# Performance work log

Measured on AMD Instinct MI355X. Metric: run time of the kernel, lower is better.

## Reference

```python
import jax, jax.numpy as jnp
import numpy as np

N_NODES = 50000
N_EDGES = 600000
D = 128
N_GRAPHS = 64


def setup_inputs() -> dict:
    key = jax.random.key(0)
    ks = jax.random.split(key, 16)
    x = jax.random.normal(ks[0], (N_NODES, D), dtype=jnp.float32)
    edge_index = jax.random.randint(ks[1], (2, N_EDGES), 0, N_NODES, dtype=jnp.int64)
    batch = jnp.sort(jax.random.randint(ks[2], (N_NODES,), 0, N_GRAPHS, dtype=jnp.int64))
    s = 1.0 / np.sqrt(D)
    def lin(k, out_d, in_d):
        return jax.random.uniform(k, (out_d, in_d), jnp.float32, -s, s)
    inp = {"x": x, "edge_index": edge_index, "batch": batch}
    for i, base in zip(range(3), (3, 6, 9)):
        inp[f"W_rel{i+1}"] = lin(ks[base], D, D)
        inp[f"b_rel{i+1}"] = jax.random.uniform(ks[base + 1], (D,), jnp.float32, -s, s)
        inp[f"W_root{i+1}"] = lin(ks[base + 2], D, D)
    s5 = 1.0 / np.sqrt(5)
    inp["W1"] = lin(ks[12], 5, D)
    inp["b1"] = jax.random.uniform(ks[13], (5,), jnp.float32, -s, s)
    inp["W2"] = jax.random.uniform(ks[14], (1, 5), jnp.float32, -s5, s5)
    inp["b2"] = jax.random.uniform(ks[15], (1,), jnp.float32, -s5, s5)
    return inp


def graph_conv(x, src, dst, W_rel, b_rel, W_root):
    # PyG GraphConv: out_i = W_root x_i + W_rel * sum_{j->i} x_j + b_rel
    agg = jax.ops.segment_sum(x[src], dst, num_segments=N_NODES)  # [N, D]
    return agg @ W_rel.T + b_rel + x @ W_root.T


def reference(x, edge_index, batch,
              W_rel1, b_rel1, W_root1,
              W_rel2, b_rel2, W_root2,
              W_rel3, b_rel3, W_root3,
              W1, b1, W2, b2):
    src, dst = edge_index[0], edge_index[1]
    h = jax.nn.relu(graph_conv(x, src, dst, W_rel1, b_rel1, W_root1))
    h = jax.nn.relu(graph_conv(h, src, dst, W_rel2, b_rel2, W_root2))
    h = graph_conv(h, src, dst, W_rel3, b_rel3, W_root3)
    # global max pool over graphs
    g = jax.ops.segment_max(h, batch, num_segments=N_GRAPHS)  # [G, D]
    out = jax.nn.relu(g @ W1.T + b1) @ W2.T + b2  # [G, 1]
    return out
```

## Files before the change

kernel.cpp:

```cpp
#include <hip/hip_runtime.h>
#include <float.h>

#define N_NODES 50000
#define N_EDGES 600000
#define D 128
#define N_GRAPHS 64
#define SCAN_T 256
#define SCAN_NBLK ((N_NODES + SCAN_T - 1) / SCAN_T)

typedef __attribute__((ext_vector_type(8))) short short8;
typedef __attribute__((ext_vector_type(4))) float floatx4;

__device__ inline float bf2f(unsigned short h) {
    return __uint_as_float((unsigned)h << 16);
}
__device__ inline unsigned short f2bf(float f) {
    unsigned u = __float_as_uint(f);
    return (unsigned short)((u + 0x7fffu + ((u >> 16) & 1u)) >> 16);
}

#define ACCQ(u, ss) {                                                            \
    int w0_ = (u).x, w1_ = (u).y, w2_ = (u).z, w3_ = (u).w;                      \
    a[ 0] += (float)(signed char)(w0_      ) * (ss);                             \
    a[ 1] += (float)(signed char)(w0_ >>  8) * (ss);                             \
    a[ 2] += (float)(signed char)(w0_ >> 16) * (ss);                             \
    a[ 3] += (float)(w0_ >> 24)              * (ss);                             \
    a[ 4] += (float)(signed char)(w1_      ) * (ss);                             \
    a[ 5] += (float)(signed char)(w1_ >>  8) * (ss);                             \
    a[ 6] += (float)(signed char)(w1_ >> 16) * (ss);                             \
    a[ 7] += (float)(w1_ >> 24)              * (ss);                             \
    a[ 8] += (float)(signed char)(w2_      ) * (ss);                             \
    a[ 9] += (float)(signed char)(w2_ >>  8) * (ss);                             \
    a[10] += (float)(signed char)(w2_ >> 16) * (ss);                             \
    a[11] += (float)(w2_ >> 24)              * (ss);                             \
    a[12] += (float)(signed char)(w3_      ) * (ss);                             \
    a[13] += (float)(signed char)(w3_ >>  8) * (ss);                             \
    a[14] += (float)(signed char)(w3_ >> 16) * (ss);                             \
    a[15] += (float)(w3_ >> 24)              * (ss); }


__global__ __launch_bounds__(256) void cast_prep(
    const float* __restrict__ x,
    unsigned short* __restrict__ xb, signed char* __restrict__ xq,
    float* __restrict__ xs,
    const float* __restrict__ Wr0, const float* __restrict__ Wo0,
    const float* __restrict__ Wr1, const float* __restrict__ Wo1,
    const float* __restrict__ Wr2, const float* __restrict__ Wo2,
    unsigned short* __restrict__ B0, unsigned short* __restrict__ B1,
    unsigned short* __restrict__ B2,
    int* __restrict__ deg, float* __restrict__ g)
{
    int t = blockIdx.x * 256 + threadIdx.x;
    if (t < N_NODES * 16) {
        int node = t >> 4, ln = t & 15;
        const float4* xr = (const float4*)(x + (size_t)node * D + ln * 8);
        float4 v0 = xr[0], v1 = xr[1];
        float v[8] = {v0.x, v0.y, v0.z, v0.w, v1.x, v1.y, v1.z, v1.w};
        float am = 0.f;
#pragma unroll
        for (int i = 0; i < 8; ++i) am = fmaxf(am, fabsf(v[i]));
#pragma unroll
        for (int m = 1; m < 16; m <<= 1) am = fmaxf(am, __shfl_xor(am, m, 16));
        float inv = (am > 0.f) ? 127.f / am : 0.f;
        short8 hb;
#pragma unroll
        for (int i = 0; i < 8; ++i) hb[i] = (short)f2bf(v[i]);
        *(short8*)(xb + (size_t)node * D + ln * 8) = hb;
        int q0 = 0, q1 = 0;
#pragma unroll
        for (int i = 0; i < 4; ++i) { int q = (int)rintf(v[i]     * inv); q0 |= (q & 0xff) << (8 * i); }
#pragma unroll
        for (int i = 0; i < 4; ++i) { int q = (int)rintf(v[4 + i] * inv); q1 |= (q & 0xff) << (8 * i); }
        int2 qp; qp.x = q0; qp.y = q1;
        *(int2*)(xq + (size_t)node * D + ln * 8) = qp;
        if (ln == 0) xs[node] = am * (1.f / 127.f);
        return;
    }
    int w = t - N_NODES * 16;
    if (w < 3 * 128 * 256) {
        int l = w >> 15;
        int r = w & 32767;
        int o = r >> 8, k = r & 255;
        const float* Wr = (l == 0) ? Wr0 : (l == 1) ? Wr1 : Wr2;
        const float* Wo = (l == 0) ? Wo0 : (l == 1) ? Wo1 : Wo2;
        unsigned short* B = (l == 0) ? B0 : (l == 1) ? B1 : B2;
        float v = (k < 128) ? Wr[o * 128 + k] : Wo[o * 128 + (k - 128)];
        B[r] = f2bf(v);
        return;
    }
    w -= 3 * 128 * 256;
    if (w < N_NODES) { deg[w] = 0; return; }
    w -= N_NODES;
    if (w < N_GRAPHS * D) g[w] = -FLT_MAX;
}


__global__ void count_deg(const int* __restrict__ ei, int* __restrict__ deg) {
    int e = blockIdx.x * 256 + threadIdx.x;
    if (e < N_EDGES) atomicAdd(&deg[ei[N_EDGES + e]], 1);
}

__global__ __launch_bounds__(SCAN_T) void block_sum(const int* __restrict__ deg,
                                                    int* __restrict__ blockSums) {
    __shared__ int s[SCAN_T];
    int tid = threadIdx.x;
    int i = blockIdx.x * SCAN_T + tid;
    s[tid] = (i < N_NODES) ? deg[i] : 0;
    __syncthreads();
    for (int off = SCAN_T / 2; off > 0; off >>= 1) {
        if (tid < off) s[tid] += s[tid + off];
        __syncthreads();
    }
    if (tid == 0) blockSums[blockIdx.x] = s[0];
}

__global__ __launch_bounds__(SCAN_T) void scan_write(const int* __restrict__ deg,
                                                     const int* __restrict__ blockSums,
                                                     int* __restrict__ row_start,
                                                     int* __restrict__ cursor) {
    __shared__ int bs[SCAN_T];
    __shared__ int s[SCAN_T];
    int tid = threadIdx.x;
    bs[tid] = (tid < SCAN_NBLK) ? blockSums[tid] : 0;
    __syncthreads();
    for (int off = 1; off < SCAN_T; off <<= 1) {
        int tt = (tid >= off) ? bs[tid - off] : 0;
        __syncthreads();
        bs[tid] += tt;
        __syncthreads();
    }
    int myOff = (blockIdx.x == 0) ? 0 : bs[blockIdx.x - 1];
    if (blockIdx.x == 0 && tid == SCAN_T - 1) row_start[N_NODES] = bs[tid];

    int i = blockIdx.x * SCAN_T + tid;
    int v = (i < N_NODES) ? deg[i] : 0;
    s[tid] = v;
    __syncthreads();
    for (int off = 1; off < SCAN_T; off <<= 1) {
        int tt = (tid >= off) ? s[tid - off] : 0;
        __syncthreads();
        s[tid] += tt;
        __syncthreads();
    }
    if (i < N_NODES) {
        int rs = myOff + s[tid] - v;
        row_start[i] = rs;
        cursor[i]    = rs;
    }
}

__global__ void fill_csr(const int* __restrict__ ei, int* __restrict__ cursor,
                         int* __restrict__ csr_src) {
    int e = blockIdx.x * 256 + threadIdx.x;
    if (e < N_EDGES) {
        int dst = ei[N_EDGES + e];
        int pos = atomicAdd(&cursor[dst], 1);
        csr_src[pos] = ei[e];
    }
}


__global__ __launch_bounds__(256) void gather_q(
    const signed char* __restrict__ xq, const float* __restrict__ xs,
    const int* __restrict__ row_start, const int* __restrict__ csr_src,
    unsigned short* __restrict__ aggb)
{
    int grp  = threadIdx.x >> 3;
    int ln   = threadIdx.x & 7;
    int node = blockIdx.x * 32 + grp;
    if (node >= N_NODES) return;
    int beg = row_start[node];
    int end = row_start[node + 1];

    float a[16];
#pragma unroll
    for (int i = 0; i < 16; ++i) a[i] = 0.f;

    for (int base = beg; base < end; base += 8) {
        int n = end - base; if (n > 8) n = 8;
        int idx = (ln < n) ? csr_src[base + ln] : 0;
        int j = 0;
        for (; j + 3 < n; j += 4) {
            int s0 = __shfl(idx, j,     8); int s1 = __shfl(idx, j + 1, 8);
            int s2 = __shfl(idx, j + 2, 8); int s3 = __shfl(idx, j + 3, 8);
            int4 u0 = *(const int4*)(xq + (size_t)s0 * D + ln * 16);
            int4 u1 = *(const int4*)(xq + (size_t)s1 * D + ln * 16);
            int4 u2 = *(const int4*)(xq + (size_t)s2 * D + ln * 16);
            int4 u3 = *(const int4*)(xq + (size_t)s3 * D + ln * 16);
            float ss0 = xs[s0], ss1 = xs[s1], ss2 = xs[s2], ss3 = xs[s3];
            ACCQ(u0, ss0); ACCQ(u1, ss1); ACCQ(u2, ss2); ACCQ(u3, ss3);
        }
        for (; j < n; ++j) {
            int s0 = __shfl(idx, j, 8);
            int4 u0 = *(const int4*)(xq + (size_t)s0 * D + ln * 16);
            float ss0 = xs[s0];
            ACCQ(u0, ss0);
        }
    }
    short8 r0, r1;
#pragma unroll
    for (int i = 0; i < 8; ++i) { r0[i] = (short)f2bf(a[i]); r1[i] = (short)f2bf(a[8 + i]); }
    *(short8*)(aggb + (size_t)node * D + ln * 16)     = r0;
    *(short8*)(aggb + (size_t)node * D + ln * 16 + 8) = r1;
}


__device__ inline void stage_b_half(unsigned short* sB, const unsigned short* __restrict__ Bb,
                                    int tid, int h) {
#pragma unroll
    for (int i = 0; i < 8; ++i) {
        int flat = tid + i * 256;
        int fi = flat >> 6, ln = flat & 63;
        int mm = ln & 15, qq = ln >> 4;
        int ksL = fi >> 3, tt = fi & 7;
        short8 v = *(const short8*)(Bb + (size_t)(tt * 16 + mm) * 256
                                    + (h * 4 + ksL) * 32 + qq * 8);
        *(short8*)(sB + (size_t)flat * 8) = v;
    }
}


struct GemmShared {
    union {
        unsigned short b[16384];
        float c[64 * 130];
    };
};

__global__ __launch_bounds__(256) void gemm_mfma(
    const unsigned short* __restrict__ aggb, const unsigned short* __restrict__ xb,
    const unsigned short* __restrict__ Bb, const float* __restrict__ bias,
    unsigned short* __restrict__ Ob, signed char* __restrict__ Oq,
    float* __restrict__ Os)
{
    __shared__ GemmShared sh;
    int tid  = threadIdx.x;
    int wave = tid >> 6;
    int lane = tid & 63;
    int m    = lane & 15;
    int quad = lane >> 4;
    int row0 = blockIdx.x * 64 + wave * 16;

    int arow = row0 + m;
    if (arow > N_NODES - 1) arow = N_NODES - 1;

    short8 af[8];
#pragma unroll
    for (int ks = 0; ks < 8; ++ks) {
        const unsigned short* Asrc = (ks < 4) ? aggb : xb;
        af[ks] = *(const short8*)(Asrc + (size_t)arow * 128 + (ks & 3) * 32 + quad * 8);
    }

    floatx4 acc[8];
#pragma unroll
    for (int t = 0; t < 8; ++t) acc[t] = (floatx4){0.f, 0.f, 0.f, 0.f};

    stage_b_half(sh.b, Bb, tid, 0);
    __syncthreads();
#pragma unroll
    for (int ksL = 0; ksL < 4; ++ksL)
#pragma unroll
        for (int t = 0; t < 8; ++t) {
            short8 b = *(const short8*)(sh.b + (size_t)((ksL * 8 + t) * 64 + lane) * 8);
            acc[t] = __builtin_amdgcn_mfma_f32_16x16x32_bf16(af[ksL], b, acc[t], 0, 0, 0);
        }
    __syncthreads();
    stage_b_half(sh.b, Bb, tid, 1);
    __syncthreads();
#pragma unroll
    for (int ksL = 0; ksL < 4; ++ksL)
#pragma unroll
        for (int t = 0; t < 8; ++t) {
            short8 b = *(const short8*)(sh.b + (size_t)((ksL * 8 + t) * 64 + lane) * 8);
            acc[t] = __builtin_amdgcn_mfma_f32_16x16x32_bf16(af[4 + ksL], b, acc[t], 0, 0, 0);
        }
    __syncthreads();

#pragma unroll
    for (int t = 0; t < 8; ++t) {
        int col = t * 16 + m;
        float bv = bias[col];
#pragma unroll
        for (int r = 0; r < 4; ++r) {
            float v = fmaxf(acc[t][r] + bv, 0.f);
            sh.c[(wave * 16 + quad * 4 + r) * 130 + col] = v;
        }
    }
    __syncthreads();

    int lr  = tid >> 2;
    int seg = tid & 3;
    int grow = blockIdx.x * 64 + lr;
    const float* cp = &sh.c[lr * 130 + seg * 32];
    float vv[32];
    float am = 0.f;
#pragma unroll
    for (int i = 0; i < 32; ++i) { vv[i] = cp[i]; am = fmaxf(am, fabsf(vv[i])); }
    am = fmaxf(am, __shfl_xor(am, 1));
    am = fmaxf(am, __shfl_xor(am, 2));
    float inv = (am > 0.f) ? 127.f / am : 0.f;

    if (grow < N_NODES) {
#pragma unroll
        for (int c8 = 0; c8 < 4; ++c8) {
            short8 hb;
#pragma unroll
            for (int i = 0; i < 8; ++i) hb[i] = (short)f2bf(vv[c8 * 8 + i]);
            *(short8*)(Ob + (size_t)grow * 128 + seg * 32 + c8 * 8) = hb;
        }
        int qd[8];
#pragma unroll
        for (int d = 0; d < 8; ++d) {
            int q = 0;
#pragma unroll
            for (int i = 0; i < 4; ++i) {
                int qq = (int)rintf(vv[d * 4 + i] * inv);
                q |= (qq & 0xff) << (8 * i);
            }
            qd[d] = q;
        }
        int4 p0; p0.x = qd[0]; p0.y = qd[1]; p0.z = qd[2]; p0.w = qd[3];
        int4 p1; p1.x = qd[4]; p1.y = qd[5]; p1.z = qd[6]; p1.w = qd[7];
        *(int4*)(Oq + (size_t)grow * 128 + seg * 32)      = p0;
        *(int4*)(Oq + (size_t)grow * 128 + seg * 32 + 16) = p1;
        if (seg == 0) Os[grow] = am * (1.f / 127.f);
    }
}


struct PoolShared {
    union {
        unsigned short b[16384];
        float c[64 * 129];
    };
};

__global__ __launch_bounds__(256) void gemm_pool(
    const unsigned short* __restrict__ aggb, const unsigned short* __restrict__ xb,
    const unsigned short* __restrict__ Bb, const float* __restrict__ bias,
    const int* __restrict__ batch, float* __restrict__ g)
{
    __shared__ PoolShared sh;
    __shared__ int bl[64];
    int tid  = threadIdx.x;
    int wave = tid >> 6;
    int lane = tid & 63;
    int m    = lane & 15;
    int quad = lane >> 4;
    int row0 = blockIdx.x * 64;

    int arow = row0 + wave * 16 + m;
    if (arow > N_NODES - 1) arow = N_NODES - 1;

    short8 af[8];
#pragma unroll
    for (int ks = 0; ks < 8; ++ks) {
        const unsigned short* Asrc = (ks < 4) ? aggb : xb;
        af[ks] = *(const short8*)(Asrc + (size_t)arow * 128 + (ks & 3) * 32 + quad * 8);
    }

    floatx4 acc[8];
#pragma unroll
    for (int t = 0; t < 8; ++t) acc[t] = (floatx4){0.f, 0.f, 0.f, 0.f};

    if (tid < 64) {
        int grow = row0 + tid;
        bl[tid] = (grow < N_NODES) ? batch[grow] : -1;
    }
    stage_b_half(sh.b, Bb, tid, 0);
    __syncthreads();
#pragma unroll
    for (int ksL = 0; ksL < 4; ++ksL)
#pragma unroll
        for (int t = 0; t < 8; ++t) {
            short8 b = *(const short8*)(sh.b + (size_t)((ksL * 8 + t) * 64 + lane) * 8);
            acc[t] = __builtin_amdgcn_mfma_f32_16x16x32_bf16(af[ksL], b, acc[t], 0, 0, 0);
        }
    __syncthreads();
    stage_b_half(sh.b, Bb, tid, 1);
    __syncthreads();
#pragma unroll
    for (int ksL = 0; ksL < 4; ++ksL)
#pragma unroll
        for (int t = 0; t < 8; ++t) {
            short8 b = *(const short8*)(sh.b + (size_t)((ksL * 8 + t) * 64 + lane) * 8);
            acc[t] = __builtin_amdgcn_mfma_f32_16x16x32_bf16(af[4 + ksL], b, acc[t], 0, 0, 0);
        }
    __syncthreads();

#pragma unroll
    for (int t = 0; t < 8; ++t) {
        int col = t * 16 + m;
        float bv = bias[col];
#pragma unroll
        for (int r = 0; r < 4; ++r)
            sh.c[(wave * 16 + quad * 4 + r) * 129 + col] = acc[t][r] + bv;
    }
    __syncthreads();

    int nvalid = min(64, N_NODES - row0);
    int b0 = bl[0], b1 = bl[nvalid - 1];
    int col  = tid & 127;
    int rbeg = (tid >> 7) * 32;
    for (int gg = b0; gg <= b1; ++gg) {
        float cur = -FLT_MAX;
#pragma unroll
        for (int r = 0; r < 32; ++r) {
            int rr = rbeg + r;
            float v = (bl[rr] == gg) ? sh.c[rr * 129 + col] : -FLT_MAX;
            cur = fmaxf(cur, v);
        }
        if (cur > -FLT_MAX) {
            float* ad = &g[gg * D + col];
            if (cur >= 0.f) atomicMax((int*)ad, __float_as_int(cur));
            else            atomicMin((unsigned int*)ad, __float_as_uint(cur));
        }
    }
}


__global__ __launch_bounds__(64) void mlp_head(const float* __restrict__ g,
                         const float* __restrict__ W1, const float* __restrict__ b1,
                         const float* __restrict__ W2, const float* __restrict__ b2,
                         float* __restrict__ out) {
    int gi = blockIdx.x;
    int lane = threadIdx.x;
    float x0 = g[gi * D + lane];
    float x1 = g[gi * D + 64 + lane];
    float o = b2[0];
#pragma unroll
    for (int j = 0; j < 5; ++j) {
        float p = x0 * W1[j * D + lane] + x1 * W1[j * D + 64 + lane];
#pragma unroll
        for (int off = 32; off > 0; off >>= 1) p += __shfl_xor(p, off, 64);
        o += fmaxf(p + b1[j], 0.f) * W2[j];
    }
    if (lane == 0) out[gi] = o;
}

extern "C" void kernel_launch(void* const* d_in, const int* in_sizes, int n_in,
                              void* d_out, int out_size, void* d_ws, size_t ws_size,
                              hipStream_t stream) {
    const float* x     = (const float*)d_in[0];
    const int*   ei    = (const int*)d_in[1];
    const int*   batch = (const int*)d_in[2];
    const float* Wrel[3]  = {(const float*)d_in[3], (const float*)d_in[6], (const float*)d_in[9]};
    const float* brel[3]  = {(const float*)d_in[4], (const float*)d_in[7], (const float*)d_in[10]};
    const float* Wroot[3] = {(const float*)d_in[5], (const float*)d_in[8], (const float*)d_in[11]};
    const float* W1 = (const float*)d_in[12];
    const float* b1 = (const float*)d_in[13];
    const float* W2 = (const float*)d_in[14];
    const float* b2 = (const float*)d_in[15];
    float* out = (float*)d_out;

    char* ws = (char*)d_ws;
    const size_t nodeB16 = (size_t)N_NODES * D * sizeof(unsigned short);
    const size_t nodeB8  = (size_t)N_NODES * D;
    unsigned short* xb   = (unsigned short*)(ws);
    unsigned short* h1b  = (unsigned short*)(ws + 1 * nodeB16);
    unsigned short* h2b  = (unsigned short*)(ws + 2 * nodeB16);
    unsigned short* aggb = (unsigned short*)(ws + 3 * nodeB16);
    char* p = ws + 4 * nodeB16;
    signed char* xq  = (signed char*)p;  p += nodeB8;
    signed char* h1q = (signed char*)p;  p += nodeB8;
    signed char* h2q = (signed char*)p;  p += nodeB8;
    float* xs  = (float*)p;  p += N_NODES * sizeof(float);
    float* h1s = (float*)p;  p += N_NODES * sizeof(float);
    float* h2s = (float*)p;  p += N_NODES * sizeof(float);
    unsigned short* Bb0 = (unsigned short*)p;   p += 128 * 256 * sizeof(unsigned short);
    unsigned short* Bb1 = (unsigned short*)p;   p += 128 * 256 * sizeof(unsigned short);
    unsigned short* Bb2 = (unsigned short*)p;   p += 128 * 256 * sizeof(unsigned short);
    float* g        = (float*)p;                p += N_GRAPHS * D * sizeof(float);
    int*   deg      = (int*)p;                  p += N_NODES * sizeof(int);
    int*   row_start= (int*)p;                  p += (N_NODES + 1) * sizeof(int);
    int*   cursor   = (int*)p;                  p += N_NODES * sizeof(int);
    int*   csr_src  = (int*)p;                  p += N_EDGES * sizeof(int);
    int*   blockSums= (int*)p;                  p += SCAN_NBLK * sizeof(int);

    const int cast_total = N_NODES * 16 + 3 * 128 * 256 + N_NODES + N_GRAPHS * D;
    cast_prep<<<(cast_total + 255) / 256, 256, 0, stream>>>(
        x, xb, xq, xs,
        Wrel[0], Wroot[0], Wrel[1], Wroot[1], Wrel[2], Wroot[2],
        Bb0, Bb1, Bb2, deg, g);

    count_deg<<<(N_EDGES + 255) / 256, 256, 0, stream>>>(ei, deg);
    block_sum<<<SCAN_NBLK, SCAN_T, 0, stream>>>(deg, blockSums);
    scan_write<<<SCAN_NBLK, SCAN_T, 0, stream>>>(deg, blockSums, row_start, cursor);
    fill_csr<<<(N_EDGES + 255) / 256, 256, 0, stream>>>(ei, cursor, csr_src);

    const int ggrid = (N_NODES + 31) / 32;
    const int mgrid = (N_NODES + 63) / 64;

    gather_q<<<ggrid, 256, 0, stream>>>(xq, xs, row_start, csr_src, aggb);
    gemm_mfma<<<mgrid, 256, 0, stream>>>(aggb, xb, Bb0, brel[0], h1b, h1q, h1s);
    gather_q<<<ggrid, 256, 0, stream>>>(h1q, h1s, row_start, csr_src, aggb);
    gemm_mfma<<<mgrid, 256, 0, stream>>>(aggb, h1b, Bb1, brel[1], h2b, h2q, h2s);
    gather_q<<<ggrid, 256, 0, stream>>>(h2q, h2s, row_start, csr_src, aggb);
    gemm_pool<<<mgrid, 256, 0, stream>>>(aggb, h2b, Bb2, brel[2], batch, g);

    mlp_head<<<N_GRAPHS, 64, 0, stream>>>(g, W1, b1, W2, b2, out);
}
```

Before: 320.4 us.

## Fuse whole GNN pipeline into one persistent cooperative kernel with grid syncs

Replaces the sequence of separate kernels (cast, degree count, scan, CSR fill, three gather/GEMM layers, pool and MLP head) with a single cooperative persistent kernel that runs the stages in grid-stride loops separated by grid.sync. It also drops the bf16 copies of the node features and dequantizes the int8 features back to bf16 for the root-term GEMM operand. The aim is to remove per-launch overhead and inter-kernel gaps. In exchange, grid-wide barriers are added, occupancy is capped by the persistent grid size, and the root term now uses int8-quantized features, which lowers accuracy.

```diff
diff --git a/kernel.cpp b/kernel.cpp
--- a/kernel.cpp
+++ b/kernel.cpp
@@ -1,12 +1,17 @@
 #include <hip/hip_runtime.h>
+#include <hip/hip_cooperative_groups.h>
 #include <float.h>
+
+namespace cg = cooperative_groups;
 
 #define N_NODES 50000
 #define N_EDGES 600000
 #define D 128
 #define N_GRAPHS 64
-#define SCAN_T 256
-#define SCAN_NBLK ((N_NODES + SCAN_T - 1) / SCAN_T)
+#define NTHR 256
+#define NG32 ((N_NODES + 31) / 32)
+#define NT64 ((N_NODES + 63) / 64)
+#define SCAN_NBLK ((N_NODES + 255) / 256)
 
 typedef __attribute__((ext_vector_type(8))) short short8;
 typedef __attribute__((ext_vector_type(4))) float floatx4;
@@ -38,180 +43,40 @@
     a[14] += (float)(signed char)(w3_ >> 16) * (ss);                             \
     a[15] += (float)(w3_ >> 24)              * (ss); }
 
-
-__global__ __launch_bounds__(256) void cast_prep(
-    const float* __restrict__ x,
-    unsigned short* __restrict__ xb, signed char* __restrict__ xq,
-    float* __restrict__ xs,
-    const float* __restrict__ Wr0, const float* __restrict__ Wo0,
-    const float* __restrict__ Wr1, const float* __restrict__ Wo1,
-    const float* __restrict__ Wr2, const float* __restrict__ Wo2,
-    unsigned short* __restrict__ B0, unsigned short* __restrict__ B1,
-    unsigned short* __restrict__ B2,
-    int* __restrict__ deg, float* __restrict__ g)
-{
-    int t = blockIdx.x * 256 + threadIdx.x;
-    if (t < N_NODES * 16) {
-        int node = t >> 4, ln = t & 15;
-        const float4* xr = (const float4*)(x + (size_t)node * D + ln * 8);
-        float4 v0 = xr[0], v1 = xr[1];
-        float v[8] = {v0.x, v0.y, v0.z, v0.w, v1.x, v1.y, v1.z, v1.w};
-        float am = 0.f;
-#pragma unroll
-        for (int i = 0; i < 8; ++i) am = fmaxf(am, fabsf(v[i]));
-#pragma unroll
-        for (int m = 1; m < 16; m <<= 1) am = fmaxf(am, __shfl_xor(am, m, 16));
-        float inv = (am > 0.f) ? 127.f / am : 0.f;
-        short8 hb;
-#pragma unroll
-        for (int i = 0; i < 8; ++i) hb[i] = (short)f2bf(v[i]);
-        *(short8*)(xb + (size_t)node * D + ln * 8) = hb;
-        int q0 = 0, q1 = 0;
-#pragma unroll
-        for (int i = 0; i < 4; ++i) { int q = (int)rintf(v[i]     * inv); q0 |= (q & 0xff) << (8 * i); }
-#pragma unroll
-        for (int i = 0; i < 4; ++i) { int q = (int)rintf(v[4 + i] * inv); q1 |= (q & 0xff) << (8 * i); }
-        int2 qp; qp.x = q0; qp.y = q1;
-        *(int2*)(xq + (size_t)node * D + ln * 8) = qp;
-        if (ln == 0) xs[node] = am * (1.f / 127.f);
-        return;
-    }
-    int w = t - N_NODES * 16;
-    if (w < 3 * 128 * 256) {
-        int l = w >> 15;
-        int r = w & 32767;
-        int o = r >> 8, k = r & 255;
-        const float* Wr = (l == 0) ? Wr0 : (l == 1) ? Wr1 : Wr2;
-        const float* Wo = (l == 0) ? Wo0 : (l == 1) ? Wo1 : Wo2;
-        unsigned short* B = (l == 0) ? B0 : (l == 1) ? B1 : B2;
-        float v = (k < 128) ? Wr[o * 128 + k] : Wo[o * 128 + (k - 128)];
-        B[r] = f2bf(v);
-        return;
-    }
-    w -= 3 * 128 * 256;
-    if (w < N_NODES) { deg[w] = 0; return; }
-    w -= N_NODES;
-    if (w < N_GRAPHS * D) g[w] = -FLT_MAX;
-}
-
-
-__global__ void count_deg(const int* __restrict__ ei, int* __restrict__ deg) {
-    int e = blockIdx.x * 256 + threadIdx.x;
-    if (e < N_EDGES) atomicAdd(&deg[ei[N_EDGES + e]], 1);
-}
-
-__global__ __launch_bounds__(SCAN_T) void block_sum(const int* __restrict__ deg,
-                                                    int* __restrict__ blockSums) {
-    __shared__ int s[SCAN_T];
-    int tid = threadIdx.x;
-    int i = blockIdx.x * SCAN_T + tid;
-    s[tid] = (i < N_NODES) ? deg[i] : 0;
-    __syncthreads();
-    for (int off = SCAN_T / 2; off > 0; off >>= 1) {
-        if (tid < off) s[tid] += s[tid + off];
-        __syncthreads();
-    }
-    if (tid == 0) blockSums[blockIdx.x] = s[0];
-}
-
-__global__ __launch_bounds__(SCAN_T) void scan_write(const int* __restrict__ deg,
-                                                     const int* __restrict__ blockSums,
-                                                     int* __restrict__ row_start,
-                                                     int* __restrict__ cursor) {
-    __shared__ int bs[SCAN_T];
-    __shared__ int s[SCAN_T];
-    int tid = threadIdx.x;
-    bs[tid] = (tid < SCAN_NBLK) ? blockSums[tid] : 0;
-    __syncthreads();
-    for (int off = 1; off < SCAN_T; off <<= 1) {
-        int tt = (tid >= off) ? bs[tid - off] : 0;
-        __syncthreads();
-        bs[tid] += tt;
-        __syncthreads();
-    }
-    int myOff = (blockIdx.x == 0) ? 0 : bs[blockIdx.x - 1];
-    if (blockIdx.x == 0 && tid == SCAN_T - 1) row_start[N_NODES] = bs[tid];
-
-    int i = blockIdx.x * SCAN_T + tid;
-    int v = (i < N_NODES) ? deg[i] : 0;
-    s[tid] = v;
-    __syncthreads();
-    for (int off = 1; off < SCAN_T; off <<= 1) {
-        int tt = (tid >= off) ? s[tid - off] : 0;
-        __syncthreads();
-        s[tid] += tt;
-        __syncthreads();
-    }
-    if (i < N_NODES) {
-        int rs = myOff + s[tid] - v;
-        row_start[i] = rs;
-        cursor[i]    = rs;
-    }
-}
-
-__global__ void fill_csr(const int* __restrict__ ei, int* __restrict__ cursor,
-                         int* __restrict__ csr_src) {
-    int e = blockIdx.x * 256 + threadIdx.x;
-    if (e < N_EDGES) {
-        int dst = ei[N_EDGES + e];
-        int pos = atomicAdd(&cursor[dst], 1);
-        csr_src[pos] = ei[e];
-    }
-}
-
-
-__global__ __launch_bounds__(256) void gather_q(
-    const signed char* __restrict__ xq, const float* __restrict__ xs,
-    const int* __restrict__ row_start, const int* __restrict__ csr_src,
-    unsigned short* __restrict__ aggb)
-{
-    int grp  = threadIdx.x >> 3;
-    int ln   = threadIdx.x & 7;
-    int node = blockIdx.x * 32 + grp;
-    if (node >= N_NODES) return;
-    int beg = row_start[node];
-    int end = row_start[node + 1];
-
-    float a[16];
-#pragma unroll
-    for (int i = 0; i < 16; ++i) a[i] = 0.f;
-
-    for (int base = beg; base < end; base += 8) {
-        int n = end - base; if (n > 8) n = 8;
-        int idx = (ln < n) ? csr_src[base + ln] : 0;
-        int j = 0;
-        for (; j + 3 < n; j += 4) {
-            int s0 = __shfl(idx, j,     8); int s1 = __shfl(idx, j + 1, 8);
-            int s2 = __shfl(idx, j + 2, 8); int s3 = __shfl(idx, j + 3, 8);
-            int4 u0 = *(const int4*)(xq + (size_t)s0 * D + ln * 16);
-            int4 u1 = *(const int4*)(xq + (size_t)s1 * D + ln * 16);
-            int4 u2 = *(const int4*)(xq + (size_t)s2 * D + ln * 16);
-            int4 u3 = *(const int4*)(xq + (size_t)s3 * D + ln * 16);
-            float ss0 = xs[s0], ss1 = xs[s1], ss2 = xs[s2], ss3 = xs[s3];
-            ACCQ(u0, ss0); ACCQ(u1, ss1); ACCQ(u2, ss2); ACCQ(u3, ss3);
-        }
-        for (; j < n; ++j) {
-            int s0 = __shfl(idx, j, 8);
-            int4 u0 = *(const int4*)(xq + (size_t)s0 * D + ln * 16);
-            float ss0 = xs[s0];
-            ACCQ(u0, ss0);
-        }
-    }
-    short8 r0, r1;
-#pragma unroll
-    for (int i = 0; i < 8; ++i) { r0[i] = (short)f2bf(a[i]); r1[i] = (short)f2bf(a[8 + i]); }
-    *(short8*)(aggb + (size_t)node * D + ln * 16)     = r0;
-    *(short8*)(aggb + (size_t)node * D + ln * 16 + 8) = r1;
-}
-
+__device__ inline short8 deq8(int2 u, float ss) {
+    short8 r;
+    r[0] = (short)f2bf((float)(signed char)(u.x      ) * ss);
+    r[1] = (short)f2bf((float)(signed char)(u.x >>  8) * ss);
+    r[2] = (short)f2bf((float)(signed char)(u.x >> 16) * ss);
+    r[3] = (short)f2bf((float)(u.x >> 24)              * ss);
+    r[4] = (short)f2bf((float)(signed char)(u.y      ) * ss);
+    r[5] = (short)f2bf((float)(signed char)(u.y >>  8) * ss);
+    r[6] = (short)f2bf((float)(signed char)(u.y >> 16) * ss);
+    r[7] = (short)f2bf((float)(u.y >> 24)              * ss);
+    return r;
+}
+
+struct Params {
+    const float* x; const int* ei; const int* batch;
+    const float* Wr0; const float* Wo0; const float* br0;
+    const float* Wr1; const float* Wo1; const float* br1;
+    const float* Wr2; const float* Wo2; const float* br2;
+    const float* W1; const float* b1; const float* W2; const float* b2;
+    float* out;
+    signed char* xq0; signed char* xq1; signed char* xq2;
+    float* xs0; float* xs1; float* xs2;
+    unsigned short* aggb;
+    unsigned short* Bb0; unsigned short* Bb1; unsigned short* Bb2;
+    float* g; int* deg; int* row_start; int* cursor; int* csr_src; int* blockSums;
+};
 
 __device__ inline void stage_b_half(unsigned short* sB, const unsigned short* __restrict__ Bb,
                                     int tid, int h) {
 #pragma unroll
     for (int i = 0; i < 8; ++i) {
         int flat = tid + i * 256;
-        int fi = flat >> 6, ln = flat & 63;
-        int mm = ln & 15, qq = ln >> 4;
+        int fi = flat >> 6, lnn = flat & 63;
+        int mm = lnn & 15, qq = lnn >> 4;
         int ksL = fi >> 3, tt = fi & 7;
         short8 v = *(const short8*)(Bb + (size_t)(tt * 16 + mm) * 256
                                     + (h * 4 + ksL) * 32 + qq * 8);
@@ -220,283 +85,361 @@
 }
 
 
-struct GemmShared {
-    union {
+__global__ __launch_bounds__(NTHR, 2) void mega(Params P) {
+    cg::grid_group grid = cg::this_grid();
+    __shared__ union U {
         unsigned short b[16384];
         float c[64 * 130];
-    };
-};
-
-__global__ __launch_bounds__(256) void gemm_mfma(
-    const unsigned short* __restrict__ aggb, const unsigned short* __restrict__ xb,
-    const unsigned short* __restrict__ Bb, const float* __restrict__ bias,
-    unsigned short* __restrict__ Ob, signed char* __restrict__ Oq,
-    float* __restrict__ Os)
-{
-    __shared__ GemmShared sh;
-    int tid  = threadIdx.x;
-    int wave = tid >> 6;
-    int lane = tid & 63;
-    int m    = lane & 15;
-    int quad = lane >> 4;
-    int row0 = blockIdx.x * 64 + wave * 16;
-
-    int arow = row0 + m;
-    if (arow > N_NODES - 1) arow = N_NODES - 1;
-
-    short8 af[8];
-#pragma unroll
-    for (int ks = 0; ks < 8; ++ks) {
-        const unsigned short* Asrc = (ks < 4) ? aggb : xb;
-        af[ks] = *(const short8*)(Asrc + (size_t)arow * 128 + (ks & 3) * 32 + quad * 8);
-    }
-
-    floatx4 acc[8];
-#pragma unroll
-    for (int t = 0; t < 8; ++t) acc[t] = (floatx4){0.f, 0.f, 0.f, 0.f};
-
-    stage_b_half(sh.b, Bb, tid, 0);
-    __syncthreads();
-#pragma unroll
-    for (int ksL = 0; ksL < 4; ++ksL)
-#pragma unroll
-        for (int t = 0; t < 8; ++t) {
-            short8 b = *(const short8*)(sh.b + (size_t)((ksL * 8 + t) * 64 + lane) * 8);
-            acc[t] = __builtin_amdgcn_mfma_f32_16x16x32_bf16(af[ksL], b, acc[t], 0, 0, 0);
-        }
-    __syncthreads();
-    stage_b_half(sh.b, Bb, tid, 1);
-    __syncthreads();
-#pragma unroll
-    for (int ksL = 0; ksL < 4; ++ksL)
-#pragma unroll
-        for (int t = 0; t < 8; ++t) {
-            short8 b = *(const short8*)(sh.b + (size_t)((ksL * 8 + t) * 64 + lane) * 8);
-            acc[t] = __builtin_amdgcn_mfma_f32_16x16x32_bf16(af[4 + ksL], b, acc[t], 0, 0, 0);
-        }
-    __syncthreads();
-
-#pragma unroll
-    for (int t = 0; t < 8; ++t) {
-        int col = t * 16 + m;
-        float bv = bias[col];
-#pragma unroll
-        for (int r = 0; r < 4; ++r) {
-            float v = fmaxf(acc[t][r] + bv, 0.f);
-            sh.c[(wave * 16 + quad * 4 + r) * 130 + col] = v;
-        }
-    }
-    __syncthreads();
-
-    int lr  = tid >> 2;
-    int seg = tid & 3;
-    int grow = blockIdx.x * 64 + lr;
-    const float* cp = &sh.c[lr * 130 + seg * 32];
-    float vv[32];
-    float am = 0.f;
-#pragma unroll
-    for (int i = 0; i < 32; ++i) { vv[i] = cp[i]; am = fmaxf(am, fabsf(vv[i])); }
-    am = fmaxf(am, __shfl_xor(am, 1));
-    am = fmaxf(am, __shfl_xor(am, 2));
-    float inv = (am > 0.f) ? 127.f / am : 0.f;
-
-    if (grow < N_NODES) {
-#pragma unroll
-        for (int c8 = 0; c8 < 4; ++c8) {
-            short8 hb;
-#pragma unroll
-            for (int i = 0; i < 8; ++i) hb[i] = (short)f2bf(vv[c8 * 8 + i]);
-            *(short8*)(Ob + (size_t)grow * 128 + seg * 32 + c8 * 8) = hb;
-        }
-        int qd[8];
-#pragma unroll
-        for (int d = 0; d < 8; ++d) {
-            int q = 0;
-#pragma unroll
-            for (int i = 0; i < 4; ++i) {
-                int qq = (int)rintf(vv[d * 4 + i] * inv);
-                q |= (qq & 0xff) << (8 * i);
+        int sc[512];
+    } sh;
+    __shared__ int bl[64];
+    const int tid  = threadIdx.x;
+    const int bid  = blockIdx.x;
+    const int nblk = gridDim.x;
+
+    {
+        const int total = N_NODES * 16 + 3 * 128 * 256 + N_NODES + N_GRAPHS * D;
+        for (int t = bid * NTHR + tid; t < total; t += nblk * NTHR) {
+            if (t < N_NODES * 16) {
+                int node = t >> 4, ln = t & 15;
+                const float4* xr = (const float4*)(P.x + (size_t)node * D + ln * 8);
+                float4 v0 = xr[0], v1 = xr[1];
+                float v[8] = {v0.x, v0.y, v0.z, v0.w, v1.x, v1.y, v1.z, v1.w};
+                float am = 0.f;
+#pragma unroll
+                for (int i = 0; i < 8; ++i) am = fmaxf(am, fabsf(v[i]));
+#pragma unroll
+                for (int mm = 1; mm < 16; mm <<= 1) am = fmaxf(am, __shfl_xor(am, mm, 16));
+                float inv = (am > 0.f) ? 127.f / am : 0.f;
+                int q0 = 0, q1 = 0;
+#pragma unroll
+                for (int i = 0; i < 4; ++i) { int q = (int)rintf(v[i]     * inv); q0 |= (q & 0xff) << (8 * i); }
+#pragma unroll
+                for (int i = 0; i < 4; ++i) { int q = (int)rintf(v[4 + i] * inv); q1 |= (q & 0xff) << (8 * i); }
+                int2 qp; qp.x = q0; qp.y = q1;
+                *(int2*)(P.xq0 + (size_t)node * D + ln * 8) = qp;
+                if (ln == 0) P.xs0[node] = am * (1.f / 127.f);
+            } else {
+                int w = t - N_NODES * 16;
+                if (w < 3 * 128 * 256) {
+                    int l = w >> 15;
+                    int r = w & 32767;
+                    int o = r >> 8, k = r & 255;
+                    const float* Wr = (l == 0) ? P.Wr0 : (l == 1) ? P.Wr1 : P.Wr2;
+                    const float* Wo = (l == 0) ? P.Wo0 : (l == 1) ? P.Wo1 : P.Wo2;
+                    unsigned short* B = (l == 0) ? P.Bb0 : (l == 1) ? P.Bb1 : P.Bb2;
+                    float v = (k < 128) ? Wr[o * 128 + k] : Wo[o * 128 + (k - 128)];
+                    B[r] = f2bf(v);
+                } else {
+                    w -= 3 * 128 * 256;
+                    if (w < N_NODES) P.deg[w] = 0;
+                    else {
+                        w -= N_NODES;
+                        if (w < N_GRAPHS * D) P.g[w] = -FLT_MAX;
+                    }
+                }
             }
-            qd[d] = q;
-        }
-        int4 p0; p0.x = qd[0]; p0.y = qd[1]; p0.z = qd[2]; p0.w = qd[3];
-        int4 p1; p1.x = qd[4]; p1.y = qd[5]; p1.z = qd[6]; p1.w = qd[7];
-        *(int4*)(Oq + (size_t)grow * 128 + seg * 32)      = p0;
-        *(int4*)(Oq + (size_t)grow * 128 + seg * 32 + 16) = p1;
-        if (seg == 0) Os[grow] = am * (1.f / 127.f);
-    }
-}
-
-
-struct PoolShared {
-    union {
-        unsigned short b[16384];
-        float c[64 * 129];
-    };
-};
-
-__global__ __launch_bounds__(256) void gemm_pool(
-    const unsigned short* __restrict__ aggb, const unsigned short* __restrict__ xb,
-    const unsigned short* __restrict__ Bb, const float* __restrict__ bias,
-    const int* __restrict__ batch, float* __restrict__ g)
-{
-    __shared__ PoolShared sh;
-    __shared__ int bl[64];
-    int tid  = threadIdx.x;
-    int wave = tid >> 6;
-    int lane = tid & 63;
-    int m    = lane & 15;
-    int quad = lane >> 4;
-    int row0 = blockIdx.x * 64;
-
-    int arow = row0 + wave * 16 + m;
-    if (arow > N_NODES - 1) arow = N_NODES - 1;
-
-    short8 af[8];
-#pragma unroll
-    for (int ks = 0; ks < 8; ++ks) {
-        const unsigned short* Asrc = (ks < 4) ? aggb : xb;
-        af[ks] = *(const short8*)(Asrc + (size_t)arow * 128 + (ks & 3) * 32 + quad * 8);
-    }
-
-    floatx4 acc[8];
-#pragma unroll
-    for (int t = 0; t < 8; ++t) acc[t] = (floatx4){0.f, 0.f, 0.f, 0.f};
-
-    if (tid < 64) {
-        int grow = row0 + tid;
-        bl[tid] = (grow < N_NODES) ? batch[grow] : -1;
-    }
-    stage_b_half(sh.b, Bb, tid, 0);
-    __syncthreads();
-#pragma unroll
-    for (int ksL = 0; ksL < 4; ++ksL)
-#pragma unroll
-        for (int t = 0; t < 8; ++t) {
-            short8 b = *(const short8*)(sh.b + (size_t)((ksL * 8 + t) * 64 + lane) * 8);
-            acc[t] = __builtin_amdgcn_mfma_f32_16x16x32_bf16(af[ksL], b, acc[t], 0, 0, 0);
-        }
-    __syncthreads();
-    stage_b_half(sh.b, Bb, tid, 1);
-    __syncthreads();
-#pragma unroll
-    for (int ksL = 0; ksL < 4; ++ksL)
-#pragma unroll
-        for (int t = 0; t < 8; ++t) {
-            short8 b = *(const short8*)(sh.b + (size_t)((ksL * 8 + t) * 64 + lane) * 8);
-            acc[t] = __builtin_amdgcn_mfma_f32_16x16x32_bf16(af[4 + ksL], b, acc[t], 0, 0, 0);
-        }
-    __syncthreads();
-
-#pragma unroll
-    for (int t = 0; t < 8; ++t) {
-        int col = t * 16 + m;
-        float bv = bias[col];
-#pragma unroll
-        for (int r = 0; r < 4; ++r)
-            sh.c[(wave * 16 + quad * 4 + r) * 129 + col] = acc[t][r] + bv;
-    }
-    __syncthreads();
-
-    int nvalid = min(64, N_NODES - row0);
-    int b0 = bl[0], b1 = bl[nvalid - 1];
-    int col  = tid & 127;
-    int rbeg = (tid >> 7) * 32;
-    for (int gg = b0; gg <= b1; ++gg) {
-        float cur = -FLT_MAX;
-#pragma unroll
-        for (int r = 0; r < 32; ++r) {
-            int rr = rbeg + r;
-            float v = (bl[rr] == gg) ? sh.c[rr * 129 + col] : -FLT_MAX;
-            cur = fmaxf(cur, v);
-        }
-        if (cur > -FLT_MAX) {
-            float* ad = &g[gg * D + col];
-            if (cur >= 0.f) atomicMax((int*)ad, __float_as_int(cur));
-            else            atomicMin((unsigned int*)ad, __float_as_uint(cur));
-        }
-    }
-}
-
-
-__global__ __launch_bounds__(64) void mlp_head(const float* __restrict__ g,
-                         const float* __restrict__ W1, const float* __restrict__ b1,
-                         const float* __restrict__ W2, const float* __restrict__ b2,
-                         float* __restrict__ out) {
-    int gi = blockIdx.x;
-    int lane = threadIdx.x;
-    float x0 = g[gi * D + lane];
-    float x1 = g[gi * D + 64 + lane];
-    float o = b2[0];
-#pragma unroll
-    for (int j = 0; j < 5; ++j) {
-        float p = x0 * W1[j * D + lane] + x1 * W1[j * D + 64 + lane];
-#pragma unroll
-        for (int off = 32; off > 0; off >>= 1) p += __shfl_xor(p, off, 64);
-        o += fmaxf(p + b1[j], 0.f) * W2[j];
-    }
-    if (lane == 0) out[gi] = o;
+        }
+    }
+    grid.sync();
+
+    for (int e = bid * NTHR + tid; e < N_EDGES; e += nblk * NTHR)
+        atomicAdd(&P.deg[P.ei[N_EDGES + e]], 1);
+    grid.sync();
+
+    for (int vb = bid; vb < SCAN_NBLK; vb += nblk) {
+        int i = vb * 256 + tid;
+        sh.sc[tid] = (i < N_NODES) ? P.deg[i] : 0;
+        __syncthreads();
+        for (int off = 128; off > 0; off >>= 1) {
+            if (tid < off) sh.sc[tid] += sh.sc[tid + off];
+            __syncthreads();
+        }
+        if (tid == 0) P.blockSums[vb] = sh.sc[0];
+        __syncthreads();
+    }
+    grid.sync();
+
+    for (int vb = bid; vb < SCAN_NBLK; vb += nblk) {
+        int* bs = sh.sc;
+        int* s  = sh.sc + 256;
+        bs[tid] = (tid < SCAN_NBLK) ? P.blockSums[tid] : 0;
+        __syncthreads();
+        for (int off = 1; off < 256; off <<= 1) {
+            int t2 = (tid >= off) ? bs[tid - off] : 0;
+            __syncthreads();
+            bs[tid] += t2;
+            __syncthreads();
+        }
+        int myOff = (vb == 0) ? 0 : bs[vb - 1];
+        if (vb == 0 && tid == 255) P.row_start[N_NODES] = bs[255];
+        int i = vb * 256 + tid;
+        int v = (i < N_NODES) ? P.deg[i] : 0;
+        s[tid] = v;
+        __syncthreads();
+        for (int off = 1; off < 256; off <<= 1) {
+            int t2 = (tid >= off) ? s[tid - off] : 0;
+            __syncthreads();
+            s[tid] += t2;
+            __syncthreads();
+        }
+        if (i < N_NODES) {
+            int rs = myOff + s[tid] - v;
+            P.row_start[i] = rs;
+            P.cursor[i]    = rs;
+        }
+        __syncthreads();
+    }
+    grid.sync();
+
+    for (int e = bid * NTHR + tid; e < N_EDGES; e += nblk * NTHR) {
+        int dst = P.ei[N_EDGES + e];
+        int pos = atomicAdd(&P.cursor[dst], 1);
+        P.csr_src[pos] = P.ei[e];
+    }
+    grid.sync();
+
+    const int wave = tid >> 6, lane = tid & 63, m = lane & 15, quad = lane >> 4;
+    const int grp = tid >> 3, ln8 = tid & 7;
+
+    for (int L = 0; L < 3; ++L) {
+        const signed char* xq = (L == 0) ? P.xq0 : (L == 1) ? P.xq1 : P.xq2;
+        const float*       xs = (L == 0) ? P.xs0 : (L == 1) ? P.xs1 : P.xs2;
+        const unsigned short* Bb = (L == 0) ? P.Bb0 : (L == 1) ? P.Bb1 : P.Bb2;
+        const float* bias = (L == 0) ? P.br0 : (L == 1) ? P.br1 : P.br2;
+        signed char* Oq = (L == 0) ? P.xq1 : P.xq2;
+        float*       Os = (L == 0) ? P.xs1 : P.xs2;
+
+        for (int vb = bid; vb < NG32; vb += nblk) {
+            int node = vb * 32 + grp;
+            if (node < N_NODES) {
+                int beg = P.row_start[node];
+                int end = P.row_start[node + 1];
+                float a[16];
+#pragma unroll
+                for (int i = 0; i < 16; ++i) a[i] = 0.f;
+                for (int base = beg; base < end; base += 8) {
+                    int n = end - base; if (n > 8) n = 8;
+                    int idx = (ln8 < n) ? P.csr_src[base + ln8] : 0;
+                    int j = 0;
+                    for (; j + 3 < n; j += 4) {
+                        int s0 = __shfl(idx, j,     8); int s1 = __shfl(idx, j + 1, 8);
+                        int s2 = __shfl(idx, j + 2, 8); int s3 = __shfl(idx, j + 3, 8);
+                        int4 u0 = *(const int4*)(xq + (size_t)s0 * D + ln8 * 16);
+                        int4 u1 = *(const int4*)(xq + (size_t)s1 * D + ln8 * 16);
+                        int4 u2 = *(const int4*)(xq + (size_t)s2 * D + ln8 * 16);
+                        int4 u3 = *(const int4*)(xq + (size_t)s3 * D + ln8 * 16);
+                        float ss0 = xs[s0], ss1 = xs[s1], ss2 = xs[s2], ss3 = xs[s3];
+                        ACCQ(u0, ss0); ACCQ(u1, ss1); ACCQ(u2, ss2); ACCQ(u3, ss3);
+                    }
+                    for (; j < n; ++j) {
+                        int s0 = __shfl(idx, j, 8);
+                        int4 u0 = *(const int4*)(xq + (size_t)s0 * D + ln8 * 16);
+                        float ss0 = xs[s0];
+                        ACCQ(u0, ss0);
+                    }
+                }
+                short8 r0, r1;
+#pragma unroll
+                for (int i = 0; i < 8; ++i) { r0[i] = (short)f2bf(a[i]); r1[i] = (short)f2bf(a[8 + i]); }
+                *(short8*)(P.aggb + (size_t)node * D + ln8 * 16)     = r0;
+                *(short8*)(P.aggb + (size_t)node * D + ln8 * 16 + 8) = r1;
+            }
+        }
+        grid.sync();
+
+        for (int vt = bid; vt < NT64; vt += nblk) {
+            int row0 = vt * 64;
+            int arow = row0 + wave * 16 + m;
+            if (arow > N_NODES - 1) arow = N_NODES - 1;
+
+            short8 afA[4];
+#pragma unroll
+            for (int ks = 0; ks < 4; ++ks)
+                afA[ks] = *(const short8*)(P.aggb + (size_t)arow * 128 + ks * 32 + quad * 8);
+
+            float fsr = xs[arow];
+            const signed char* xr = xq + (size_t)arow * 128 + quad * 8;
+            short8 afX[4];
+            afX[0] = deq8(*(const int2*)(xr),      fsr);
+            afX[1] = deq8(*(const int2*)(xr + 32), fsr);
+            afX[2] = deq8(*(const int2*)(xr + 64), fsr);
+            afX[3] = deq8(*(const int2*)(xr + 96), fsr);
+
+            if (L == 2 && tid < 64) {
+                int grow = row0 + tid;
+                bl[tid] = (grow < N_NODES) ? P.batch[grow] : -1;
+            }
+
+            floatx4 acc[8];
+#pragma unroll
+            for (int t = 0; t < 8; ++t) acc[t] = (floatx4){0.f, 0.f, 0.f, 0.f};
+
+            stage_b_half(sh.b, Bb, tid, 0);
+            __syncthreads();
+#pragma unroll
+            for (int ksL = 0; ksL < 4; ++ksL)
+#pragma unroll
+                for (int t = 0; t < 8; ++t) {
+                    short8 b = *(const short8*)(sh.b + (size_t)((ksL * 8 + t) * 64 + lane) * 8);
+                    acc[t] = __builtin_amdgcn_mfma_f32_16x16x32_bf16(afA[ksL], b, acc[t], 0, 0, 0);
+                }
+            __syncthreads();
+            stage_b_half(sh.b, Bb, tid, 1);
+            __syncthreads();
+#pragma unroll
+            for (int ksL = 0; ksL < 4; ++ksL)
+#pragma unroll
+                for (int t = 0; t < 8; ++t) {
+                    short8 b = *(const short8*)(sh.b + (size_t)((ksL * 8 + t) * 64 + lane) * 8);
+                    acc[t] = __builtin_amdgcn_mfma_f32_16x16x32_bf16(afX[ksL], b, acc[t], 0, 0, 0);
+                }
+            __syncthreads();
+
+            if (L < 2) {
+#pragma unroll
+                for (int t = 0; t < 8; ++t) {
+                    int col = t * 16 + m;
+                    float bv = bias[col];
+#pragma unroll
+                    for (int r = 0; r < 4; ++r)
+                        sh.c[(wave * 16 + quad * 4 + r) * 130 + col] = fmaxf(acc[t][r] + bv, 0.f);
+                }
+                __syncthreads();
+
+                int lr  = tid >> 2;
+                int seg = tid & 3;
+                int grow = row0 + lr;
+                const float* cp = &sh.c[lr * 130 + seg * 32];
+                float vv[32];
+                float am = 0.f;
+#pragma unroll
+                for (int i = 0; i < 32; ++i) { vv[i] = cp[i]; am = fmaxf(am, fabsf(vv[i])); }
+                am = fmaxf(am, __shfl_xor(am, 1));
+                am = fmaxf(am, __shfl_xor(am, 2));
+                float inv = (am > 0.f) ? 127.f / am : 0.f;
+
+                if (grow < N_NODES) {
+                    int qd[8];
+#pragma unroll
+                    for (int d = 0; d < 8; ++d) {
+                        int q = 0;
+#pragma unroll
+                        for (int i = 0; i < 4; ++i) {
+                            int qq = (int)rintf(vv[d * 4 + i] * inv);
+                            q |= (qq & 0xff) << (8 * i);
+                        }
+                        qd[d] = q;
+                    }
+                    int4 p0; p0.x = qd[0]; p0.y = qd[1]; p0.z = qd[2]; p0.w = qd[3];
+                    int4 p1; p1.x = qd[4]; p1.y = qd[5]; p1.z = qd[6]; p1.w = qd[7];
+                    *(int4*)(Oq + (size_t)grow * 128 + seg * 32)      = p0;
+                    *(int4*)(Oq + (size_t)grow * 128 + seg * 32 + 16) = p1;
+                    if (seg == 0) Os[grow] = am * (1.f / 127.f);
+                }
+                __syncthreads();
+            } else {
+#pragma unroll
+                for (int t = 0; t < 8; ++t) {
+                    int col = t * 16 + m;
+                    float bv = bias[col];
+#pragma unroll
+                    for (int r = 0; r < 4; ++r)
+                        sh.c[(wave * 16 + quad * 4 + r) * 130 + col] = acc[t][r] + bv;
+                }
+                __syncthreads();
+
+                int nvalid = min(64, N_NODES - row0);
+                int b0 = bl[0], b1 = bl[nvalid - 1];
+                int col  = tid & 127;
+                int rbeg = (tid >> 7) * 32;
+                for (int gg = b0; gg <= b1; ++gg) {
+                    float cur = -FLT_MAX;
+#pragma unroll
+                    for (int r = 0; r < 32; ++r) {
+                        int rr = rbeg + r;
+                        float v = (bl[rr] == gg) ? sh.c[rr * 130 + col] : -FLT_MAX;
+                        cur = fmaxf(cur, v);
+                    }
+                    if (cur > -FLT_MAX) {
+                        float* ad = &P.g[gg * D + col];
+                        if (cur >= 0.f) atomicMax((int*)ad, __float_as_int(cur));
+                        else            atomicMin((unsigned int*)ad, __float_as_uint(cur));
+                    }
+                }
+                __syncthreads();
+            }
+        }
+        grid.sync();
+    }
+
+    if (bid < N_GRAPHS && tid < 64) {
+        int gi = bid;
+        float x0 = P.g[gi * D + tid];
+        float x1 = P.g[gi * D + 64 + tid];
+        float o = P.b2[0];
+#pragma unroll
+        for (int j = 0; j < 5; ++j) {
+            float p = x0 * P.W1[j * D + tid] + x1 * P.W1[j * D + 64 + tid];
+#pragma unroll
+            for (int off = 32; off > 0; off >>= 1) p += __shfl_xor(p, off, 64);
+            o += fmaxf(p + P.b1[j], 0.f) * P.W2[j];
+        }
+        if (tid == 0) P.out[gi] = o;
+    }
 }
 
 extern "C" void kernel_launch(void* const* d_in, const int* in_sizes, int n_in,
                               void* d_out, int out_size, void* d_ws, size_t ws_size,
                               hipStream_t stream) {
-    const float* x     = (const float*)d_in[0];
-    const int*   ei    = (const int*)d_in[1];
-    const int*   batch = (const int*)d_in[2];
-    const float* Wrel[3]  = {(const float*)d_in[3], (const float*)d_in[6], (const float*)d_in[9]};
-    const float* brel[3]  = {(const float*)d_in[4], (const float*)d_in[7], (const float*)d_in[10]};
-    const float* Wroot[3] = {(const float*)d_in[5], (const float*)d_in[8], (const float*)d_in[11]};
-    const float* W1 = (const float*)d_in[12];
-    const float* b1 = (const float*)d_in[13];
-    const float* W2 = (const float*)d_in[14];
-    const float* b2 = (const float*)d_in[15];
-    float* out = (float*)d_out;
+    Params P;
+    P.x     = (const float*)d_in[0];
+    P.ei    = (const int*)d_in[1];
+    P.batch = (const int*)d_in[2];
+    P.Wr0 = (const float*)d_in[3];  P.br0 = (const float*)d_in[4];  P.Wo0 = (const float*)d_in[5];
+    P.Wr1 = (const float*)d_in[6];  P.br1 = (const float*)d_in[7];  P.Wo1 = (const float*)d_in[8];
+    P.Wr2 = (const float*)d_in[9];  P.br2 = (const float*)d_in[10]; P.Wo2 = (const float*)d_in[11];
+    P.W1 = (const float*)d_in[12]; P.b1 = (const float*)d_in[13];
+    P.W2 = (const float*)d_in[14]; P.b2 = (const float*)d_in[15];
+    P.out = (float*)d_out;
 
     char* ws = (char*)d_ws;
-    const size_t nodeB16 = (size_t)N_NODES * D * sizeof(unsigned short);
-    const size_t nodeB8  = (size_t)N_NODES * D;
-    unsigned short* xb   = (unsigned short*)(ws);
-    unsigned short* h1b  = (unsigned short*)(ws + 1 * nodeB16);
-    unsigned short* h2b  = (unsigned short*)(ws + 2 * nodeB16);
-    unsigned short* aggb = (unsigned short*)(ws + 3 * nodeB16);
-    char* p = ws + 4 * nodeB16;
-    signed char* xq  = (signed char*)p;  p += nodeB8;
-    signed char* h1q = (signed char*)p;  p += nodeB8;
-    signed char* h2q = (signed char*)p;  p += nodeB8;
-    float* xs  = (float*)p;  p += N_NODES * sizeof(float);
-    float* h1s = (float*)p;  p += N_NODES * sizeof(float);
-    float* h2s = (float*)p;  p += N_NODES * sizeof(float);
-    unsigned short* Bb0 = (unsigned short*)p;   p += 128 * 256 * sizeof(unsigned short);
-    unsigned short* Bb1 = (unsigned short*)p;   p += 128 * 256 * sizeof(unsigned short);
-    unsigned short* Bb2 = (unsigned short*)p;   p += 128 * 256 * sizeof(unsigned short);
-    float* g        = (float*)p;                p += N_GRAPHS * D * sizeof(float);
-    int*   deg      = (int*)p;                  p += N_NODES * sizeof(int);
-    int*   row_start= (int*)p;                  p += (N_NODES + 1) * sizeof(int);
-    int*   cursor   = (int*)p;                  p += N_NODES * sizeof(int);
-    int*   csr_src  = (int*)p;                  p += N_EDGES * sizeof(int);
-    int*   blockSums= (int*)p;                  p += SCAN_NBLK * sizeof(int);
-
-    const int cast_total = N_NODES * 16 + 3 * 128 * 256 + N_NODES + N_GRAPHS * D;
-    cast_prep<<<(cast_total + 255) / 256, 256, 0, stream>>>(
-        x, xb, xq, xs,
-        Wrel[0], Wroot[0], Wrel[1], Wroot[1], Wrel[2], Wroot[2],
-        Bb0, Bb1, Bb2, deg, g);
-
-    count_deg<<<(N_EDGES + 255) / 256, 256, 0, stream>>>(ei, deg);
-    block_sum<<<SCAN_NBLK, SCAN_T, 0, stream>>>(deg, blockSums);
-    scan_write<<<SCAN_NBLK, SCAN_T, 0, stream>>>(deg, blockSums, row_start, cursor);
-    fill_csr<<<(N_EDGES + 255) / 256, 256, 0, stream>>>(ei, cursor, csr_src);
-
-    const int ggrid = (N_NODES + 31) / 32;
-    const int mgrid = (N_NODES + 63) / 64;
-
-    gather_q<<<ggrid, 256, 0, stream>>>(xq, xs, row_start, csr_src, aggb);
-    gemm_mfma<<<mgrid, 256, 0, stream>>>(aggb, xb, Bb0, brel[0], h1b, h1q, h1s);
-    gather_q<<<ggrid, 256, 0, stream>>>(h1q, h1s, row_start, csr_src, aggb);
-    gemm_mfma<<<mgrid, 256, 0, stream>>>(aggb, h1b, Bb1, brel[1], h2b, h2q, h2s);
-    gather_q<<<ggrid, 256, 0, stream>>>(h2q, h2s, row_start, csr_src, aggb);
-    gemm_pool<<<mgrid, 256, 0, stream>>>(aggb, h2b, Bb2, brel[2], batch, g);
-
-    mlp_head<<<N_GRAPHS, 64, 0, stream>>>(g, W1, b1, W2, b2, out);
-}
+    const size_t nodeB8 = (size_t)N_NODES * D;
+    P.xq0 = (signed char*)(ws);
+    P.xq1 = (signed char*)(ws + 1 * nodeB8);
+    P.xq2 = (signed char*)(ws + 2 * nodeB8);
+    char* p = ws + 3 * nodeB8;
+    P.aggb = (unsigned short*)p;  p += (size_t)N_NODES * D * sizeof(unsigned short);
+    P.xs0 = (float*)p;  p += N_NODES * sizeof(float);
+    P.xs1 = (float*)p;  p += N_NODES * sizeof(float);
+    P.xs2 = (float*)p;  p += N_NODES * sizeof(float);
+    P.Bb0 = (unsigned short*)p;   p += 128 * 256 * sizeof(unsigned short);
+    P.Bb1 = (unsigned short*)p;   p += 128 * 256 * sizeof(unsigned short);
+    P.Bb2 = (unsigned short*)p;   p += 128 * 256 * sizeof(unsigned short);
+    P.g         = (float*)p;      p += N_GRAPHS * D * sizeof(float);
+    P.deg       = (int*)p;        p += N_NODES * sizeof(int);
+    P.row_start = (int*)p;        p += (N_NODES + 1) * sizeof(int);
+    P.cursor    = (int*)p;        p += N_NODES * sizeof(int);
+    P.csr_src   = (int*)p;        p += N_EDGES * sizeof(int);
+    P.blockSums = (int*)p;        p += SCAN_NBLK * sizeof(int);
+
+    static int nblk = 0;
+    if (nblk == 0) {
+        int per_cu = 0;
+        if (hipOccupancyMaxActiveBlocksPerMultiprocessor(&per_cu, mega, NTHR, 0)
+                != hipSuccess || per_cu < 1)
+            per_cu = 1;
+        int ncu = 0;
+        int dev = 0;
+        hipGetDevice(&dev);
+        if (hipDeviceGetAttribute(&ncu, hipDeviceAttributeMultiprocessorCount, dev)
+                != hipSuccess || ncu < 1)
+            ncu = 256;
+        nblk = per_cu * ncu;
+        if (nblk < 64) nblk = 64;
+    }
+
+    void* args[] = { &P };
+    hipLaunchCooperativeKernel((const void*)mega, dim3(nblk), dim3(NTHR),
+                               args, 0, stream);
+}
```

New measurement: 731.4 us. 128% more time.
